# Optimization experiments

Hardware: AMD Instinct MI355X
Metric: run time of the kernel (lower is better)

Reference implementation:

```python
import jax, jax.numpy as jnp
import numpy as np

CHEB_K = 3  # from init_kwargs

def _layernorm(v, g, b, eps=1e-12):
    mu = jnp.mean(v, axis=-1, keepdims=True)
    var = jnp.var(v, axis=-1, keepdims=True)  # biased, matches torch LayerNorm
    return (v - mu) * jax.lax.rsqrt(var + eps) * g + b

def setup_inputs() -> dict:
    key = jax.random.key(0)
    ks = jax.random.split(key, 5)
    B, N, D_IN, D_OUT, E = 64, 2048, 64, 64, 16
    return {
        "x": jax.random.normal(ks[0], (B, N, D_IN), dtype=jnp.float32),
        "node_embeddings": jax.random.normal(ks[1], (N, E), dtype=jnp.float32),
        "time_embeddings": jax.random.normal(ks[2], (E,), dtype=jnp.float32),
        "weights_pool": jax.random.normal(ks[3], (E, CHEB_K, D_IN, D_OUT), dtype=jnp.float32) * 0.1,
        "bias_pool": jax.random.normal(ks[4], (E, D_OUT), dtype=jnp.float32) * 0.1,
        "ln_gamma": jnp.ones((E,), dtype=jnp.float32),
        "ln_beta": jnp.zeros((E,), dtype=jnp.float32),
    }

def reference(x, node_embeddings, time_embeddings, weights_pool, bias_pool, ln_gamma, ln_beta):
    N = node_embeddings.shape[0]
    # dropout in eval mode -> identity
    ne = _layernorm(node_embeddings + time_embeddings[None, :], ln_gamma, ln_beta)  # [N,E]
    supports0 = jax.nn.softmax(ne @ ne.T, axis=1)  # [N,N]
    support_set = [jnp.eye(N, dtype=x.dtype), supports0]
    for _ in range(2, CHEB_K):
        support_set.append(2.0 * supports0 @ support_set[-1] - support_set[-2])
    supports = jnp.stack(support_set, axis=0)  # [K,N,N]
    weights = jnp.einsum('nd,dkio->nkio', ne, weights_pool)  # [N,K,I,O]
    bias = ne @ bias_pool  # [N,O]
    x_g = jnp.einsum('knm,bmc->bnkc', supports, x)  # [B,N,K,I]
    return jnp.einsum('bnki,nkio->bno', x_g, weights) + bias  # [B,N,O]
```

## Files before the change

kernel.cpp:

```cpp
#include <hip/hip_runtime.h>
#include <stdint.h>

typedef unsigned short u16;
typedef __attribute__((ext_vector_type(8))) short   bf16x8;
typedef __attribute__((ext_vector_type(4))) float   f32x4;
typedef __attribute__((ext_vector_type(4))) u16     u16x4;
typedef __attribute__((ext_vector_type(8))) u16     u16x8;

#define NN 2048
#define BB 64
#define DD 64
#define XSTRIDE (NN*DD)

__device__ __forceinline__ float bf2f(u16 u) {
    union { unsigned int i; float f; } v; v.i = ((unsigned int)u) << 16; return v.f;
}
__device__ __forceinline__ u16 f2bf(float f) {
    union { float f; unsigned int i; } v; v.f = f;
    unsigned int u = v.i;
    return (u16)((u + 0x7fffu + ((u >> 16) & 1u)) >> 16);
}

typedef __attribute__((address_space(3))) unsigned int lds_u32_t;
typedef const __attribute__((address_space(1))) unsigned int g_u32_t;
__device__ __forceinline__ void gload_lds16(const void* g, void* l) {
    __builtin_amdgcn_global_load_lds((g_u32_t*)(uintptr_t)g, (lds_u32_t*)(uintptr_t)l, 16, 0, 0);
}

__global__ __launch_bounds__(256) void k_ln(const float* __restrict__ nodee,
                                            const float* __restrict__ timee,
                                            const float* __restrict__ gamma,
                                            const float* __restrict__ beta,
                                            float* __restrict__ ne,
                                            u16* __restrict__ neb) {
    int n = blockIdx.x * 256 + threadIdx.x;
    float v[16]; float mu = 0.f;
    const float4* p = (const float4*)(nodee + (long)n * 16);
#pragma unroll
    for (int i = 0; i < 4; i++) {
        float4 q = p[i];
        v[i*4+0]=q.x; v[i*4+1]=q.y; v[i*4+2]=q.z; v[i*4+3]=q.w;
    }
#pragma unroll
    for (int e = 0; e < 16; e++) { v[e] += timee[e]; mu += v[e]; }
    mu *= (1.f/16.f);
    float var = 0.f;
#pragma unroll
    for (int e = 0; e < 16; e++) { float d = v[e]-mu; var += d*d; }
    var *= (1.f/16.f);
    float rs = rsqrtf(var + 1e-12f);
    float4* o = (float4*)(ne + (long)n * 16);
    u16x8 nb[2];
#pragma unroll
    for (int i = 0; i < 4; i++) {
        float4 q;
        q.x = (v[i*4+0]-mu)*rs*gamma[i*4+0] + beta[i*4+0];
        q.y = (v[i*4+1]-mu)*rs*gamma[i*4+1] + beta[i*4+1];
        q.z = (v[i*4+2]-mu)*rs*gamma[i*4+2] + beta[i*4+2];
        q.w = (v[i*4+3]-mu)*rs*gamma[i*4+3] + beta[i*4+3];
        o[i] = q;
        nb[i>>1][(i&1)*4+0] = f2bf(q.x); nb[i>>1][(i&1)*4+1] = f2bf(q.y);
        nb[i>>1][(i&1)*4+2] = f2bf(q.z); nb[i>>1][(i&1)*4+3] = f2bf(q.w);
    }
    u16x8 z;
#pragma unroll
    for (int j = 0; j < 8; j++) z[j] = 0;
    u16x8* ob = (u16x8*)&neb[(long)n * 32];
    ob[0] = nb[0]; ob[1] = nb[1]; ob[2] = z; ob[3] = z;
}

__global__ __launch_bounds__(256) void k_wperm(const float* __restrict__ wp,
                                               u16* __restrict__ wpP) {
    int j = blockIdx.x * 256 + threadIdx.x;
    int o = j / 192, ki = j - o * 192;
    int src = ki * 64 + o;
    u16x8 ov[4];
#pragma unroll
    for (int e = 0; e < 16; e++) ov[e>>3][e&7] = f2bf(wp[(long)e*12288 + src]);
#pragma unroll
    for (int e = 0; e < 8; e++) { ov[2][e] = 0; ov[3][e] = 0; }
    u16x8* dst = (u16x8*)&wpP[(long)j * 32];
    dst[0]=ov[0]; dst[1]=ov[1]; dst[2]=ov[2]; dst[3]=ov[3];
}

__global__ __launch_bounds__(256) void k_softmax(const float* __restrict__ ne,
                                                 u16* __restrict__ S) {
    __shared__ float row[2048];
    __shared__ float red[8];
    int n = blockIdx.x, t = threadIdx.x;
    int wave = t >> 6, lane = t & 63;
    f32x4 nev[4];
#pragma unroll
    for (int i = 0; i < 4; i++) nev[i] = *(const f32x4*)&ne[n*16 + i*4];
    float lmax = -1e30f;
    for (int m = t; m < 2048; m += 256) {
        const f32x4* p = (const f32x4*)&ne[m*16];
        f32x4 d4 = nev[0]*p[0] + nev[1]*p[1] + nev[2]*p[2] + nev[3]*p[3];
        float d = d4[0]+d4[1]+d4[2]+d4[3];
        row[m] = d;
        lmax = fmaxf(lmax, d);
    }
#pragma unroll
    for (int off = 32; off > 0; off >>= 1) lmax = fmaxf(lmax, __shfl_xor(lmax, off));
    if (lane == 0) red[wave] = lmax;
    __syncthreads();
    float gmax = fmaxf(fmaxf(red[0], red[1]), fmaxf(red[2], red[3]));
    float lsum = 0.f;
    for (int m = t; m < 2048; m += 256) {
        float ev = __expf(row[m] - gmax);
        row[m] = ev;
        lsum += ev;
    }
#pragma unroll
    for (int off = 32; off > 0; off >>= 1) lsum += __shfl_xor(lsum, off);
    __syncthreads();
    if (lane == 0) red[wave] = lsum;
    __syncthreads();
    float inv = 1.f / (red[0]+red[1]+red[2]+red[3]);
    for (int m = t; m < 2048; m += 256)
        S[(long)n*2048 + m] = f2bf(row[m] * inv);
}

__global__ __launch_bounds__(256) void k_permute(const float* __restrict__ x,
                                                 u16* __restrict__ Xpt) {
    __shared__ u16 T[64][72];
    int bid = blockIdx.x;
    int b = bid >> 5, m0 = (bid & 31) * 64;
    int t = threadIdx.x;
#pragma unroll
    for (int it = 0; it < 4; it++) {
        int fi = it*256 + t;
        int row = fi >> 4, c4 = (fi & 15) * 4;
        float4 v = *(const float4*)&x[(long)b*XSTRIDE + (m0+row)*64 + c4];
        T[c4+0][row] = f2bf(v.x); T[c4+1][row] = f2bf(v.y);
        T[c4+2][row] = f2bf(v.z); T[c4+3][row] = f2bf(v.w);
    }
    __syncthreads();
#pragma unroll
    for (int it = 0; it < 2; it++) {
        int ch = it*256 + t;
        int c = ch >> 3, m8 = (ch & 7) * 8;
        u16x8 v = *(const u16x8*)&T[c][m8];
        *(u16x8*)&Xpt[(long)(b*64 + c)*2048 + m0 + m8] = v;
    }
}

__global__ __launch_bounds__(256) void k_gemm_bt(const u16* __restrict__ A,
                                                 const u16* __restrict__ Bt,
                                                 u16* __restrict__ C,
                                                 int M, int Ncols, int K) {
    __shared__ __align__(16) u16 As[128*32];
    __shared__ __align__(16) u16 Bs[128*32];
    const int t = threadIdx.x;
    const int wave = t >> 6, lane = t & 63;
    const int l15 = lane & 15, lhi = lane >> 4;
    const int m0 = blockIdx.y * 128;
    const int n0 = blockIdx.x * 128;
    const int wr = wave >> 1, wc = wave & 1;
    f32x4 acc[4][4] = {};
    const int srow = t >> 2;
    const int sk = (t & 3) * 8;
    const u16* gA = A + (long)(m0 + srow) * K + sk;
    const u16* gB = Bt + (long)(n0 + srow) * K + sk;
    const long half = (long)64 * K;
    u16* lA = As + wave * 512;
    u16* lB = Bs + wave * 512;
    const int aoff = (wr*64 + l15)*32 + lhi*8;
    const int boff = (wc*64 + l15)*32 + lhi*8;
    for (int k0 = 0; k0 < K; k0 += 32) {
        gload_lds16(gA + k0,        lA);
        gload_lds16(gA + k0 + half, lA + 2048);
        gload_lds16(gB + k0,        lB);
        gload_lds16(gB + k0 + half, lB + 2048);
        __syncthreads();
        bf16x8 af[4], bv[4];
#pragma unroll
        for (int m = 0; m < 4; m++) af[m] = *(const bf16x8*)&As[aoff + m*512];
#pragma unroll
        for (int q = 0; q < 4; q++) bv[q] = *(const bf16x8*)&Bs[boff + q*512];
#pragma unroll
        for (int m = 0; m < 4; m++)
#pragma unroll
            for (int q = 0; q < 4; q++)
                acc[m][q] = __builtin_amdgcn_mfma_f32_16x16x32_bf16(af[m], bv[q], acc[m][q], 0, 0, 0);
        __syncthreads();
    }
#pragma unroll
    for (int m = 0; m < 4; m++) {
        int row = m0 + wr*64 + m*16 + lhi*4;
#pragma unroll
        for (int q = 0; q < 4; q++) {
            int col = n0 + wc*64 + q*16 + l15;
#pragma unroll
            for (int r = 0; r < 4; r++)
                C[(long)(row + r) * Ncols + col] = f2bf(acc[m][q][r]);
        }
    }
}

__global__ __launch_bounds__(256, 1) void k_gemm_big(const u16* __restrict__ A,
                                                     const u16* __restrict__ Bt,
                                                     u16* __restrict__ C,
                                                     u16* __restrict__ Ct,
                                                     int M, int Ncols, int K) {
    __shared__ __align__(16) u16 LB[73728];
    const int t = threadIdx.x;
    const int wave = t >> 6, lane = t & 63;
    const int l15 = lane & 15, lhi = lane >> 4;
    const int nwg = gridDim.x * gridDim.y;
    const int wgid = blockIdx.y * gridDim.x + blockIdx.x;
    const int swz = (wgid & 7) * (nwg >> 3) + (wgid >> 3);
    const int by = swz / gridDim.x, bx = swz - (swz / gridDim.x) * gridDim.x;
    const int m0 = by * 128, n0 = bx * 256;
    const int wr = wave >> 1, wc = wave & 1;
    const int NT = K >> 6;
    f32x4 acc[4][8] = {};

    const int srow = t >> 3;
    const int sswz = ((t & 7) ^ (srow & 7)) * 8;
    const u16* gA0 = A  + (long)(m0 + srow) * K + sswz;
    const u16* gB0 = Bt + (long)(n0 + srow) * K + sswz;
    const long rA = (long)32 * K;
    const int ldsW = wave * 512;

    int curA = 0,     nxtA = 8192,          tgtA = 16384;
    int curB = 24576, nxtB = 24576 + 16384, tgtB = 24576 + 32768;

#pragma unroll
    for (int r = 0; r < 4; r++) gload_lds16(gA0 + r*rA,      &LB[curA + r*2048 + ldsW]);
#pragma unroll
    for (int r = 0; r < 8; r++) gload_lds16(gB0 + r*rA,      &LB[curB + r*2048 + ldsW]);
#pragma unroll
    for (int r = 0; r < 4; r++) gload_lds16(gA0 + r*rA + 64, &LB[nxtA + r*2048 + ldsW]);
#pragma unroll
    for (int r = 0; r < 8; r++) gload_lds16(gB0 + r*rA + 64, &LB[nxtB + r*2048 + ldsW]);
    asm volatile("s_waitcnt vmcnt(12)" ::: "memory");
    __builtin_amdgcn_s_barrier();
    asm volatile("" ::: "memory");

    const int arow = wr*64 + l15, aswz = arow & 7, abase = arow * 64;
    const int bcol = wc*128 + l15, bswz = bcol & 7, bbase = bcol * 64;

#pragma unroll 1
    for (int tt = 0; tt < NT; tt++) {
        const bool stg = (tt + 2 < NT);
        const long ko2 = (long)((tt + 2) << 6);
        {
            const int sa = (lhi ^ aswz) * 8, sb = (lhi ^ bswz) * 8;
            bf16x8 af[4], bv[8];
#pragma unroll
            for (int m = 0; m < 4; m++) af[m] = *(const bf16x8*)&LB[curA + abase + m*1024 + sa];
#pragma unroll
            for (int q = 0; q < 8; q++) bv[q] = *(const bf16x8*)&LB[curB + bbase + q*1024 + sb];
            if (stg) {
                gload_lds16(gA0 + 0*rA + ko2, &LB[tgtA + 0*2048 + ldsW]);
                gload_lds16(gA0 + 1*rA + ko2, &LB[tgtA + 1*2048 + ldsW]);
                gload_lds16(gA0 + 2*rA + ko2, &LB[tgtA + 2*2048 + ldsW]);
                gload_lds16(gA0 + 3*rA + ko2, &LB[tgtA + 3*2048 + ldsW]);
                gload_lds16(gB0 + 0*rA + ko2, &LB[tgtB + 0*2048 + ldsW]);
                gload_lds16(gB0 + 1*rA + ko2, &LB[tgtB + 1*2048 + ldsW]);
            }
            __builtin_amdgcn_s_setprio(1);
#pragma unroll
            for (int m = 0; m < 4; m++)
#pragma unroll
                for (int q = 0; q < 8; q++)
                    acc[m][q] = __builtin_amdgcn_mfma_f32_16x16x32_bf16(af[m], bv[q], acc[m][q], 0, 0, 0);
            __builtin_amdgcn_s_setprio(0);
        }
        {
            const int sa = ((4 + lhi) ^ aswz) * 8, sb = ((4 + lhi) ^ bswz) * 8;
            bf16x8 af[4], bv[8];
#pragma unroll
            for (int m = 0; m < 4; m++) af[m] = *(const bf16x8*)&LB[curA + abase + m*1024 + sa];
#pragma unroll
            for (int q = 0; q < 8; q++) bv[q] = *(const bf16x8*)&LB[curB + bbase + q*1024 + sb];
            if (stg) {
                gload_lds16(gB0 + 2*rA + ko2, &LB[tgtB + 2*2048 + ldsW]);
                gload_lds16(gB0 + 3*rA + ko2, &LB[tgtB + 3*2048 + ldsW]);
                gload_lds16(gB0 + 4*rA + ko2, &LB[tgtB + 4*2048 + ldsW]);
                gload_lds16(gB0 + 5*rA + ko2, &LB[tgtB + 5*2048 + ldsW]);
                gload_lds16(gB0 + 6*rA + ko2, &LB[tgtB + 6*2048 + ldsW]);
                gload_lds16(gB0 + 7*rA + ko2, &LB[tgtB + 7*2048 + ldsW]);
            }
            __builtin_amdgcn_s_setprio(1);
#pragma unroll
            for (int m = 0; m < 4; m++)
#pragma unroll
                for (int q = 0; q < 8; q++)
                    acc[m][q] = __builtin_amdgcn_mfma_f32_16x16x32_bf16(af[m], bv[q], acc[m][q], 0, 0, 0);
            __builtin_amdgcn_s_setprio(0);
        }
        asm volatile("" ::: "memory");
        if (stg)                asm volatile("s_waitcnt vmcnt(12)" ::: "memory");
        else if (tt + 1 < NT)   asm volatile("s_waitcnt vmcnt(0)" ::: "memory");
        if (tt + 1 < NT) {
            __builtin_amdgcn_s_barrier();
            asm volatile("" ::: "memory");
        }
        int ta = curA; curA = nxtA; nxtA = tgtA; tgtA = ta;
        int tb = curB; curB = nxtB; nxtB = tgtB; tgtB = tb;
    }
#pragma unroll
    for (int m = 0; m < 4; m++) {
        int row = m0 + wr*64 + m*16 + lhi*4;
#pragma unroll
        for (int q = 0; q < 8; q++) {
            int col = n0 + wc*128 + q*16 + l15;
#pragma unroll
            for (int r = 0; r < 4; r++)
                C[(long)(row + r) * Ncols + col] = f2bf(acc[m][q][r]);
        }
    }
    if (Ct != nullptr) {
        __syncthreads();
#pragma unroll
        for (int m = 0; m < 4; m++) {
            int rowb = wr*64 + m*16 + lhi*4;
#pragma unroll
            for (int q = 0; q < 8; q++) {
                int col = wc*128 + q*16 + l15;
                u16x4 p;
                p[0]=f2bf(acc[m][q][0]); p[1]=f2bf(acc[m][q][1]);
                p[2]=f2bf(acc[m][q][2]); p[3]=f2bf(acc[m][q][3]);
                *(u16x4*)&LB[col*136 + rowb] = p;
            }
        }
        __syncthreads();
        const int j16 = t >> 4, ch = (t & 15) * 8;
#pragma unroll
        for (int p = 0; p < 16; p++) {
            int j = p*16 + j16;
            u16x8 v = *(const u16x8*)&LB[j*136 + ch];
            *(u16x8*)&Ct[(long)(n0 + j)*M + m0 + ch] = v;
        }
    }
}

__global__ __launch_bounds__(256) void k_final(const float* __restrict__ x,
                                               const u16* __restrict__ Y1,
                                               const u16* __restrict__ Y2,
                                               const u16* __restrict__ Wt,
                                               const float* __restrict__ ne,
                                               const float* __restrict__ bp,
                                               float* __restrict__ out) {
    __shared__ __align__(16) u16 Al[64*200];
    __shared__ __align__(16) u16 Wl[64*200];
    __shared__ float biasl[64];
    int n = blockIdx.x;
    int t = threadIdx.x;
    int wave = t >> 6, lane = t & 63;
    int l15 = lane & 15, lhi = lane >> 4;
#pragma unroll
    for (int it = 0; it < 6; it++) {
        int ch = it*256 + t;
        int o = ch / 24, kl = (ch % 24) * 8;
        u16x8 v = *(const u16x8*)&Wt[(long)n*12288 + ch*8];
        *(u16x8*)&Wl[o*200 + kl] = v;
    }
    float xs[16];
#pragma unroll
    for (int it = 0; it < 4; it++) {
        int fi = it*256 + t;
        int b = fi >> 4, i4 = (fi & 15) * 4;
        float4 v = *(const float4*)&x[(long)b*XSTRIDE + n*64 + i4];
        xs[it*4+0]=v.x; xs[it*4+1]=v.y; xs[it*4+2]=v.z; xs[it*4+3]=v.w;
        u16x4 p; p[0]=f2bf(v.x); p[1]=f2bf(v.y); p[2]=f2bf(v.z); p[3]=f2bf(v.w);
        *(u16x4*)&Al[b*200 + i4] = p;
    }
#pragma unroll
    for (int it = 0; it < 2; it++) {
        int ch = it*256 + t;
        int b = ch >> 3, i8 = (ch & 7)*8;
        u16x8 v = *(const u16x8*)&Y1[(long)n*4096 + ch*8];
        *(u16x8*)&Al[b*200 + 64 + i8] = v;
    }
#pragma unroll
    for (int it = 0; it < 4; it++) {
        int fi = it*256 + t;
        int b = fi >> 4, i4 = (fi & 15)*4;
        u16x4 y = *(const u16x4*)&Y2[(long)n*4096 + fi*4];
        u16x4 p;
#pragma unroll
        for (int j = 0; j < 4; j++) p[j] = f2bf(2.f*bf2f(y[j]) - xs[it*4+j]);
        *(u16x4*)&Al[b*200 + 128 + i4] = p;
    }
    if (t < 64) {
        float s = 0.f;
#pragma unroll
        for (int e = 0; e < 16; e++) s += ne[n*16+e] * bp[e*64 + t];
        biasl[t] = s;
    }
    __syncthreads();
    f32x4 acc[4] = {};
#pragma unroll
    for (int kk = 0; kk < 6; kk++) {
        bf16x8 bv = *(const bf16x8*)&Wl[(wave*16 + l15)*200 + kk*32 + lhi*8];
#pragma unroll
        for (int m = 0; m < 4; m++) {
            bf16x8 av = *(const bf16x8*)&Al[(m*16 + l15)*200 + kk*32 + lhi*8];
            acc[m] = __builtin_amdgcn_mfma_f32_16x16x32_bf16(av, bv, acc[m], 0, 0, 0);
        }
    }
    int o = wave*16 + l15;
    float bias = biasl[o];
#pragma unroll
    for (int m = 0; m < 4; m++) {
        int brow = m*16 + lhi*4;
#pragma unroll
        for (int r = 0; r < 4; r++)
            out[(long)(brow + r)*XSTRIDE + n*64 + o] = acc[m][r] + bias;
    }
}

extern "C" void kernel_launch(void* const* d_in, const int* in_sizes, int n_in,
                              void* d_out, int out_size, void* d_ws, size_t ws_size,
                              hipStream_t stream) {
    const float* x     = (const float*)d_in[0];
    const float* nodee = (const float*)d_in[1];
    const float* timee = (const float*)d_in[2];
    const float* wp    = (const float*)d_in[3];
    const float* bp    = (const float*)d_in[4];
    const float* gamma = (const float*)d_in[5];
    const float* beta  = (const float*)d_in[6];
    float* out = (float*)d_out;

    char* ws = (char*)d_ws;
    float* ne  = (float*)(ws);
    u16* S     = (u16*)(ws + 131072);
    u16* Xpt   = (u16*)(ws + 8519680);
    u16* Y1    = (u16*)(ws + 25296896);
    u16* Y1t   = (u16*)(ws + 42074112);
    u16* Y2    = (u16*)(ws + 58851328);
    u16* Wt    = (u16*)(ws + 75628544);
    u16* neb   = (u16*)(ws + 58851328);
    u16* wpP   = (u16*)(ws + 58851328 + 131072);
    if (ws_size < (size_t)125960192) return;

    k_ln      <<<8,    256, 0, stream>>>(nodee, timee, gamma, beta, ne, neb);
    k_wperm   <<<48,   256, 0, stream>>>(wp, wpP);
    k_gemm_bt <<<dim3(96,16), 256, 0, stream>>>(neb, wpP, Wt, 2048, 12288, 32);
    k_softmax <<<2048, 256, 0, stream>>>(ne, S);
    k_permute <<<2048, 256, 0, stream>>>(x, Xpt);
    k_gemm_big<<<dim3(16,16), 256, 0, stream>>>(S, Xpt, Y1, Y1t, 2048, 4096, 2048);
    k_gemm_big<<<dim3(16,16), 256, 0, stream>>>(S, Y1t, Y2, (u16*)nullptr, 2048, 4096, 2048);
    k_final   <<<2048, 256, 0, stream>>>(x, Y1, Y2, Wt, ne, bp, out);
}
```

Baseline: 154.0 us.

## Use 8 waves per block in big GEMM with barrier-interleaved load/MFMA phases

The 128x256 GEMM tile is now split across 8 waves, each owning a 64x64 sub-tile, instead of 4 waves with 64x128 each. That halves the accumulator registers per wave and doubles the number of waves resident on the CU. The K-step is split into four MFMA phases separated by block barriers, with LDS fragment reads and global-to-LDS prefetches staggered between them. The aim is better overlap of memory traffic and matrix work. The extra barriers per iteration add synchronisation cost, and the 8-wave layout may change LDS bank behaviour.

```diff
diff --git a/kernel.cpp b/kernel.cpp
--- a/kernel.cpp
+++ b/kernel.cpp
@@ -198,7 +198,7 @@
     }
 }
 
-__global__ __launch_bounds__(256, 1) void k_gemm_big(const u16* __restrict__ A,
+__global__ __launch_bounds__(512, 2) void k_gemm_big(const u16* __restrict__ A,
                                                      const u16* __restrict__ Bt,
                                                      u16* __restrict__ C,
                                                      u16* __restrict__ Ct,
@@ -210,91 +210,112 @@
     const int nwg = gridDim.x * gridDim.y;
     const int wgid = blockIdx.y * gridDim.x + blockIdx.x;
     const int swz = (wgid & 7) * (nwg >> 3) + (wgid >> 3);
-    const int by = swz / gridDim.x, bx = swz - (swz / gridDim.x) * gridDim.x;
+    const int by = swz / gridDim.x, bx = swz - by * gridDim.x;
     const int m0 = by * 128, n0 = bx * 256;
-    const int wr = wave >> 1, wc = wave & 1;
+    const int wr = wave >> 2, wc = wave & 3;
     const int NT = K >> 6;
-    f32x4 acc[4][8] = {};
+    f32x4 acc[4][4] = {};
 
     const int srow = t >> 3;
     const int sswz = ((t & 7) ^ (srow & 7)) * 8;
     const u16* gA0 = A  + (long)(m0 + srow) * K + sswz;
     const u16* gB0 = Bt + (long)(n0 + srow) * K + sswz;
-    const long rA = (long)32 * K;
+    const long rP = (long)64 * K;
     const int ldsW = wave * 512;
 
-    int curA = 0,     nxtA = 8192,          tgtA = 16384;
-    int curB = 24576, nxtB = 24576 + 16384, tgtB = 24576 + 32768;
-
-#pragma unroll
-    for (int r = 0; r < 4; r++) gload_lds16(gA0 + r*rA,      &LB[curA + r*2048 + ldsW]);
-#pragma unroll
-    for (int r = 0; r < 8; r++) gload_lds16(gB0 + r*rA,      &LB[curB + r*2048 + ldsW]);
-#pragma unroll
-    for (int r = 0; r < 4; r++) gload_lds16(gA0 + r*rA + 64, &LB[nxtA + r*2048 + ldsW]);
-#pragma unroll
-    for (int r = 0; r < 8; r++) gload_lds16(gB0 + r*rA + 64, &LB[nxtB + r*2048 + ldsW]);
-    asm volatile("s_waitcnt vmcnt(12)" ::: "memory");
+    int curA = 0,     nxtA = 8192,  tgtA = 16384;
+    int curB = 24576, nxtB = 40960, tgtB = 57344;
+
+    gload_lds16(gA0,           &LB[curA + 0*4096 + ldsW]);
+    gload_lds16(gA0 + rP,      &LB[curA + 1*4096 + ldsW]);
+#pragma unroll
+    for (int r = 0; r < 4; r++) gload_lds16(gB0 + r*rP,      &LB[curB + r*4096 + ldsW]);
+    gload_lds16(gA0 + 64,      &LB[nxtA + 0*4096 + ldsW]);
+    gload_lds16(gA0 + rP + 64, &LB[nxtA + 1*4096 + ldsW]);
+#pragma unroll
+    for (int r = 0; r < 4; r++) gload_lds16(gB0 + r*rP + 64, &LB[nxtB + r*4096 + ldsW]);
+    asm volatile("s_waitcnt vmcnt(6)" ::: "memory");
     __builtin_amdgcn_s_barrier();
     asm volatile("" ::: "memory");
 
-    const int arow = wr*64 + l15, aswz = arow & 7, abase = arow * 64;
-    const int bcol = wc*128 + l15, bswz = bcol & 7, bbase = bcol * 64;
+    const int rsw = l15 & 7;
+    const int sw0 = (lhi ^ rsw) * 8;
+    const int sw1 = ((4 + lhi) ^ rsw) * 8;
+    const int abase = (wr*64 + l15) * 64;
+    const int bbase = (wc*64 + l15) * 64;
 
 #pragma unroll 1
     for (int tt = 0; tt < NT; tt++) {
         const bool stg = (tt + 2 < NT);
         const long ko2 = (long)((tt + 2) << 6);
-        {
-            const int sa = (lhi ^ aswz) * 8, sb = (lhi ^ bswz) * 8;
-            bf16x8 af[4], bv[8];
-#pragma unroll
-            for (int m = 0; m < 4; m++) af[m] = *(const bf16x8*)&LB[curA + abase + m*1024 + sa];
-#pragma unroll
-            for (int q = 0; q < 8; q++) bv[q] = *(const bf16x8*)&LB[curB + bbase + q*1024 + sb];
-            if (stg) {
-                gload_lds16(gA0 + 0*rA + ko2, &LB[tgtA + 0*2048 + ldsW]);
-                gload_lds16(gA0 + 1*rA + ko2, &LB[tgtA + 1*2048 + ldsW]);
-                gload_lds16(gA0 + 2*rA + ko2, &LB[tgtA + 2*2048 + ldsW]);
-                gload_lds16(gA0 + 3*rA + ko2, &LB[tgtA + 3*2048 + ldsW]);
-                gload_lds16(gB0 + 0*rA + ko2, &LB[tgtB + 0*2048 + ldsW]);
-                gload_lds16(gB0 + 1*rA + ko2, &LB[tgtB + 1*2048 + ldsW]);
-            }
-            __builtin_amdgcn_s_setprio(1);
-#pragma unroll
-            for (int m = 0; m < 4; m++)
-#pragma unroll
-                for (int q = 0; q < 8; q++)
-                    acc[m][q] = __builtin_amdgcn_mfma_f32_16x16x32_bf16(af[m], bv[q], acc[m][q], 0, 0, 0);
-            __builtin_amdgcn_s_setprio(0);
-        }
-        {
-            const int sa = ((4 + lhi) ^ aswz) * 8, sb = ((4 + lhi) ^ bswz) * 8;
-            bf16x8 af[4], bv[8];
-#pragma unroll
-            for (int m = 0; m < 4; m++) af[m] = *(const bf16x8*)&LB[curA + abase + m*1024 + sa];
-#pragma unroll
-            for (int q = 0; q < 8; q++) bv[q] = *(const bf16x8*)&LB[curB + bbase + q*1024 + sb];
-            if (stg) {
-                gload_lds16(gB0 + 2*rA + ko2, &LB[tgtB + 2*2048 + ldsW]);
-                gload_lds16(gB0 + 3*rA + ko2, &LB[tgtB + 3*2048 + ldsW]);
-                gload_lds16(gB0 + 4*rA + ko2, &LB[tgtB + 4*2048 + ldsW]);
-                gload_lds16(gB0 + 5*rA + ko2, &LB[tgtB + 5*2048 + ldsW]);
-                gload_lds16(gB0 + 6*rA + ko2, &LB[tgtB + 6*2048 + ldsW]);
-                gload_lds16(gB0 + 7*rA + ko2, &LB[tgtB + 7*2048 + ldsW]);
-            }
-            __builtin_amdgcn_s_setprio(1);
-#pragma unroll
-            for (int m = 0; m < 4; m++)
-#pragma unroll
-                for (int q = 0; q < 8; q++)
-                    acc[m][q] = __builtin_amdgcn_mfma_f32_16x16x32_bf16(af[m], bv[q], acc[m][q], 0, 0, 0);
-            __builtin_amdgcn_s_setprio(0);
-        }
+        bf16x8 af0[4], af1[4], bv0[4], bv1[4];
+#pragma unroll
+        for (int m = 0; m < 4; m++) af0[m] = *(const bf16x8*)&LB[curA + abase + m*1024 + sw0];
+        bv0[0] = *(const bf16x8*)&LB[curB + bbase + 0*1024 + sw0];
+        bv0[1] = *(const bf16x8*)&LB[curB + bbase + 1*1024 + sw0];
+        if (stg) {
+            gload_lds16(gA0 + ko2,      &LB[tgtA + 0*4096 + ldsW]);
+            gload_lds16(gA0 + rP + ko2, &LB[tgtA + 1*4096 + ldsW]);
+        }
+        __builtin_amdgcn_s_barrier();
+        asm volatile("s_waitcnt lgkmcnt(0)" ::: "memory");
+        __builtin_amdgcn_s_setprio(1);
+#pragma unroll
+        for (int m = 0; m < 4; m++)
+#pragma unroll
+            for (int q = 0; q < 2; q++)
+                acc[m][q] = __builtin_amdgcn_mfma_f32_16x16x32_bf16(af0[m], bv0[q], acc[m][q], 0, 0, 0);
+        __builtin_amdgcn_s_setprio(0);
+        __builtin_amdgcn_s_barrier();
+        bv0[2] = *(const bf16x8*)&LB[curB + bbase + 2*1024 + sw0];
+        bv0[3] = *(const bf16x8*)&LB[curB + bbase + 3*1024 + sw0];
+        if (stg) {
+            gload_lds16(gB0 + ko2,      &LB[tgtB + 0*4096 + ldsW]);
+            gload_lds16(gB0 + rP + ko2, &LB[tgtB + 1*4096 + ldsW]);
+        }
+        __builtin_amdgcn_s_barrier();
+        asm volatile("s_waitcnt lgkmcnt(0)" ::: "memory");
+        __builtin_amdgcn_s_setprio(1);
+#pragma unroll
+        for (int m = 0; m < 4; m++)
+#pragma unroll
+            for (int q = 2; q < 4; q++)
+                acc[m][q] = __builtin_amdgcn_mfma_f32_16x16x32_bf16(af0[m], bv0[q], acc[m][q], 0, 0, 0);
+        __builtin_amdgcn_s_setprio(0);
+        __builtin_amdgcn_s_barrier();
+#pragma unroll
+        for (int m = 0; m < 4; m++) af1[m] = *(const bf16x8*)&LB[curA + abase + m*1024 + sw1];
+        bv1[0] = *(const bf16x8*)&LB[curB + bbase + 0*1024 + sw1];
+        bv1[1] = *(const bf16x8*)&LB[curB + bbase + 1*1024 + sw1];
+        if (stg) {
+            gload_lds16(gB0 + 2*rP + ko2, &LB[tgtB + 2*4096 + ldsW]);
+            gload_lds16(gB0 + 3*rP + ko2, &LB[tgtB + 3*4096 + ldsW]);
+        }
+        __builtin_amdgcn_s_barrier();
+        asm volatile("s_waitcnt lgkmcnt(0)" ::: "memory");
+        __builtin_amdgcn_s_setprio(1);
+#pragma unroll
+        for (int m = 0; m < 4; m++)
+#pragma unroll
+            for (int q = 0; q < 2; q++)
+                acc[m][q] = __builtin_amdgcn_mfma_f32_16x16x32_bf16(af1[m], bv1[q], acc[m][q], 0, 0, 0);
+        __builtin_amdgcn_s_setprio(0);
+        __builtin_amdgcn_s_barrier();
+        bv1[2] = *(const bf16x8*)&LB[curB + bbase + 2*1024 + sw1];
+        bv1[3] = *(const bf16x8*)&LB[curB + bbase + 3*1024 + sw1];
+        __builtin_amdgcn_s_barrier();
+        asm volatile("s_waitcnt lgkmcnt(0)" ::: "memory");
+        __builtin_amdgcn_s_setprio(1);
+#pragma unroll
+        for (int m = 0; m < 4; m++)
+#pragma unroll
+            for (int q = 2; q < 4; q++)
+                acc[m][q] = __builtin_amdgcn_mfma_f32_16x16x32_bf16(af1[m], bv1[q], acc[m][q], 0, 0, 0);
+        __builtin_amdgcn_s_setprio(0);
         asm volatile("" ::: "memory");
-        if (stg)                asm volatile("s_waitcnt vmcnt(12)" ::: "memory");
-        else if (tt + 1 < NT)   asm volatile("s_waitcnt vmcnt(0)" ::: "memory");
         if (tt + 1 < NT) {
+            if (stg) asm volatile("s_waitcnt vmcnt(6)" ::: "memory");
+            else     asm volatile("s_waitcnt vmcnt(0)" ::: "memory");
             __builtin_amdgcn_s_barrier();
             asm volatile("" ::: "memory");
         }
@@ -305,8 +326,8 @@
     for (int m = 0; m < 4; m++) {
         int row = m0 + wr*64 + m*16 + lhi*4;
 #pragma unroll
-        for (int q = 0; q < 8; q++) {
-            int col = n0 + wc*128 + q*16 + l15;
+        for (int q = 0; q < 4; q++) {
+            int col = n0 + wc*64 + q*16 + l15;
 #pragma unroll
             for (int r = 0; r < 4; r++)
                 C[(long)(row + r) * Ncols + col] = f2bf(acc[m][q][r]);
@@ -318,8 +339,8 @@
         for (int m = 0; m < 4; m++) {
             int rowb = wr*64 + m*16 + lhi*4;
 #pragma unroll
-            for (int q = 0; q < 8; q++) {
-                int col = wc*128 + q*16 + l15;
+            for (int q = 0; q < 4; q++) {
+                int col = wc*64 + q*16 + l15;
                 u16x4 p;
                 p[0]=f2bf(acc[m][q][0]); p[1]=f2bf(acc[m][q][1]);
                 p[2]=f2bf(acc[m][q][2]); p[3]=f2bf(acc[m][q][3]);
@@ -329,8 +350,8 @@
         __syncthreads();
         const int j16 = t >> 4, ch = (t & 15) * 8;
 #pragma unroll
-        for (int p = 0; p < 16; p++) {
-            int j = p*16 + j16;
+        for (int p = 0; p < 8; p++) {
+            int j = p*32 + j16;
             u16x8 v = *(const u16x8*)&LB[j*136 + ch];
             *(u16x8*)&Ct[(long)(n0 + j)*M + m0 + ch] = v;
         }
@@ -442,7 +463,7 @@
     k_gemm_bt <<<dim3(96,16), 256, 0, stream>>>(neb, wpP, Wt, 2048, 12288, 32);
     k_softmax <<<2048, 256, 0, stream>>>(ne, S);
     k_permute <<<2048, 256, 0, stream>>>(x, Xpt);
-    k_gemm_big<<<dim3(16,16), 256, 0, stream>>>(S, Xpt, Y1, Y1t, 2048, 4096, 2048);
-    k_gemm_big<<<dim3(16,16), 256, 0, stream>>>(S, Y1t, Y2, (u16*)nullptr, 2048, 4096, 2048);
+    k_gemm_big<<<dim3(16,16), 512, 0, stream>>>(S, Xpt, Y1, Y1t, 2048, 4096, 2048);
+    k_gemm_big<<<dim3(16,16), 512, 0, stream>>>(S, Y1t, Y2, (u16*)nullptr, 2048, 4096, 2048);
     k_final   <<<2048, 256, 0, stream>>>(x, Y1, Y2, Wt, ne, bp, out);
 }
```

New measurement: 155.9 us. About the same (+1.3%).
